# Performance work log

Measured on AMD Instinct MI355X. Metric: run time of the kernel, lower is better.

The kernel has to match this reference:

```python
import jax, jax.numpy as jnp
import numpy as np

K = 10  # neighbors (k = min(k, N-1); N=4096 >> 10)
EPS = 1e-5  # InstanceNorm eps (torch default)


def knn_idx(coords, k):
    # coords: [B,3,N] -> indices of k nearest neighbors (excluding self) [B,N,k]
    pts = coords.transpose(0, 2, 1)  # [B,N,3]
    sq = jnp.sum(pts * pts, axis=-1)  # [B,N]
    dist = sq[:, :, None] + sq[:, None, :] - 2.0 * jnp.einsum('bnc,bmc->bnm', pts, pts)
    dist = jnp.clip(dist, 1e-12)
    _, idx = jax.lax.top_k(-dist, k + 1)  # ascending distance, sorted
    return idx[:, :, 1:]  # drop self


def graph_feature(idx, feats):
    # feats: [B,C,N], idx: [B,N,k] -> [B,2C,N,k] = [center, neighbor-center]
    neigh = jax.vmap(lambda f, i: f[:, i])(feats, idx)  # [B,C,N,k]
    center = jnp.broadcast_to(feats[..., None], neigh.shape)
    return jnp.concatenate([center, neigh - center], axis=1)


def instance_norm(x):
    # x: [B,C,N,k]; normalize over spatial dims per (batch, channel), no affine
    mu = jnp.mean(x, axis=(2, 3), keepdims=True)
    var = jnp.var(x, axis=(2, 3), keepdims=True)
    return (x - mu) * jax.lax.rsqrt(var + EPS)


def lrelu(x):
    return jnp.where(x >= 0, x, 0.2 * x)


def setup_inputs() -> dict:
    key = jax.random.key(0)
    k1, k2, k3, k4, k5 = jax.random.split(key, 5)
    B, C, N = 4, 128, 4096
    coords = jax.random.normal(k1, (B, 3, N), dtype=jnp.float32)
    features = jax.random.normal(k2, (B, C, N), dtype=jnp.float32)
    W1 = jax.random.normal(k3, (C, 2 * C), dtype=jnp.float32) * 0.05
    W2 = jax.random.normal(k4, (2 * C, 2 * C), dtype=jnp.float32) * 0.05
    W3 = jax.random.normal(k5, (C, 4 * C), dtype=jnp.float32) * 0.05
    return {"coords": coords, "features": features, "W1": W1, "W2": W2, "W3": W3}


def reference(coords, features, W1, W2, W3):
    idx = knn_idx(coords, K)  # same KNN graph used by both EdgeConv stages
    x0 = features  # [B,C,N]
    # stage 1: EdgeConv C -> C
    g1 = graph_feature(idx, x0)  # [B,2C,N,k]
    x1 = lrelu(instance_norm(jnp.einsum('oc,bcnk->bonk', W1, g1)))
    x1 = jnp.max(x1, axis=-1)  # [B,C,N]
    # stage 2: EdgeConv C -> 2C
    g2 = graph_feature(idx, x1)  # [B,2C,N,k] (input C, cat -> 2C)
    x2 = lrelu(instance_norm(jnp.einsum('oc,bcnk->bonk', W2, g2)))
    x2 = jnp.max(x2, axis=-1)  # [B,2C,N]
    # fuse: [x0,x1,x2] -> 4C -> C via conv1x1 + InstanceNorm (spatial = N)
    x3 = jnp.concatenate([x0, x1, x2], axis=1)  # [B,4C,N]
    x3 = jnp.einsum('oc,bcn->bon', W3, x3)[..., None]  # [B,C,N,1]
    x3 = lrelu(instance_norm(x3))[..., 0]  # [B,C,N]
    return x3
```

## Files before the change

kernel.cpp:

```cpp
#include <hip/hip_runtime.h>
#include <math.h>
#include <stdint.h>

#define NB 4
#define NC 128
#define NP 4096
#define KNN 10


__device__ __forceinline__ uint16_t f2bf(float f) {
  uint32_t u = __float_as_uint(f);
  u += 0x7fffu + ((u >> 16) & 1u);
  return (uint16_t)(u >> 16);
}
__device__ __forceinline__ float bf2f(uint16_t h) {
  return __uint_as_float(((uint32_t)h) << 16);
}

__device__ __forceinline__ void async16(const void* g, void* l) {
  __builtin_amdgcn_global_load_lds(
      (const __attribute__((address_space(1))) unsigned int*)g,
      (__attribute__((address_space(3))) unsigned int*)l,
      16, 0, 0);
}

__device__ __forceinline__ uint32_t fsort(float f) {
  uint32_t u = __float_as_uint(f);
  return (u & 0x80000000u) ? ~u : (u | 0x80000000u);
}
__device__ __forceinline__ float funsort(uint32_t k) {
  uint32_t u = (k & 0x80000000u) ? (k & 0x7fffffffu) : ~k;
  return __uint_as_float(u);
}

typedef __bf16 bf16x8 __attribute__((ext_vector_type(8)));
typedef float f32x4 __attribute__((ext_vector_type(4)));

__global__ void k_prep(const float* __restrict__ W1, const float* __restrict__ W2,
                       const float* __restrict__ W3, const float* __restrict__ coords,
                       uint16_t* __restrict__ W1cat, uint16_t* __restrict__ W2cat,
                       uint16_t* __restrict__ W3b,
                       float* __restrict__ stats, float4* __restrict__ pts4) {
  int t = blockIdx.x * 256 + threadIdx.x;
  if (t < 32768) {
    int o = t >> 7, c = t & 127;
    float v;
    if (o < 128) v = W1[o * 256 + c] - W1[o * 256 + 128 + c];
    else         v = W1[(o - 128) * 256 + 128 + c];
    W1cat[t] = f2bf(v);
  } else if (t < 98304) {
    int t2 = t - 32768;
    int o = t2 >> 7, c = t2 & 127;
    float v;
    if (o < 256) v = W2[o * 256 + c] - W2[o * 256 + 128 + c];
    else         v = W2[(o - 256) * 256 + 128 + c];
    W2cat[t2] = f2bf(v);
  } else if (t < 163840) {
    int t2 = t - 98304;
    W3b[t2] = f2bf(W3[t2]);
  } else if (t < 163840 + 8192) {
    stats[t - 163840] = 0.f;
  } else if (t < 163840 + 8192 + 16384) {
    int t2 = t - 163840 - 8192;
    int b = t2 >> 12, n = t2 & 4095;
    const float* cb = coords + b * 12288;
    float x = cb[n], y = cb[4096 + n], z = cb[8192 + n];
    float w = fmaf(x, x, fmaf(y, y, z * z));
    pts4[t2] = make_float4(x, y, z, w);
  }
}

__global__ void k_trans_feat(const float* __restrict__ feat, uint16_t* __restrict__ Xcat) {
  __shared__ float tile[32][33];
  int bid = blockIdx.x;
  int b = bid >> 9;
  int r = bid & 511;
  int n0 = (r >> 2) << 5;
  int c0 = (r & 3) << 5;
  int tx = threadIdx.x & 31, ty = threadIdx.x >> 5;
#pragma unroll
  for (int i = 0; i < 4; i++) {
    int c = c0 + ty + i * 8;
    tile[ty + i * 8][tx] = feat[(b * 128 + c) * 4096 + n0 + tx];
  }
  __syncthreads();
#pragma unroll
  for (int i = 0; i < 4; i++) {
    int n = n0 + ty + i * 8;
    Xcat[((b * 4096 + n) * 512) + c0 + tx] = f2bf(tile[tx][ty + i * 8]);
  }
}

__global__ void k_knn_thr(const float4* __restrict__ pts4, float* __restrict__ candd) {
  int L = blockIdx.x;
  int ch = L & 7;
  int qb = (L >> 3) & 15;
  int b = L >> 7;
  int m0 = ch << 7;
  const float4* pb = pts4 + b * 4096;
  int t = threadIdx.x;
  int q = (qb << 8) + t;
  float4 qp = pb[q];
  float d10[10];
#pragma unroll
  for (int i = 0; i < 10; i++) d10[i] = 1e30f;
#pragma unroll 2
  for (int mm = 0; mm < 128; mm++) {
    int m = m0 + mm;
    float4 p = pb[m];
    float dot = fmaf(qp.x, p.x, fmaf(qp.y, p.y, qp.z * p.z));
    float s = qp.w + p.w;
    float d = fmaf(-2.f, dot, s);
    d = (m == q) ? 1e30f : d;
    if (d < d10[9]) {
      float carry = d;
#pragma unroll
      for (int i = 0; i < 10; i++) {
        float lo = fminf(d10[i], carry);
        carry = fmaxf(d10[i], carry);
        d10[i] = lo;
      }
    }
  }
  int row = b * 4096 + q;
#pragma unroll
  for (int i = 0; i < 10; i++) candd[row * 80 + ch * 10 + i] = d10[i];
}

__global__ void k_knn_merge(const float* __restrict__ candd, float* __restrict__ tq) {
  int gw = blockIdx.x * 4 + (threadIdx.x >> 6);
  int l = threadIdx.x & 63;
  const float* cp = candd + (size_t)gw * 80;
  uint32_t k0 = fsort(cp[l]);
  uint32_t k1 = (l < 16) ? fsort(cp[64 + l]) : 0xFFFFFFFFu;
  uint32_t g = 0;
#pragma unroll
  for (int it = 0; it < 10; it++) {
    uint32_t m = k0 < k1 ? k0 : k1;
#pragma unroll
    for (int s = 1; s < 64; s <<= 1) {
      uint32_t o = __shfl_xor(m, s);
      m = o < m ? o : m;
    }
    g = m;
    if (it < 9) {
      if (k0 == m) k0 = 0xFFFFFFFFu;
      else if (k1 == m) k1 = 0xFFFFFFFFu;
    }
  }
  if (l == 0) tq[gw] = funsort(g);
}

#define CFCAP 112
#define DMARGIN 1e-3f
__global__ __launch_bounds__(256) void k_knn_cf(
    const float4* __restrict__ pts4, const float* __restrict__ tq,
    int* __restrict__ idxout) {
  __shared__ int candi[8 * CFCAP];
  __shared__ int ccnt[8];
  int blk = blockIdx.x;
  int b = blk >> 9;
  int qg = blk & 511;
  int t = threadIdx.x;
  if (t < 8) ccnt[t] = 0;
  const float4* pb = pts4 + b * 4096;
  int qbase = qg * 8;
  float q2x[8], q2y[8], q2z[8], rhs[8];
#pragma unroll
  for (int j = 0; j < 8; j++) {
    float4 qp = pb[qbase + j];
    q2x[j] = -2.f * qp.x; q2y[j] = -2.f * qp.y; q2z[j] = -2.f * qp.z;
    rhs[j] = tq[b * 4096 + qbase + j] + DMARGIN - qp.w;
  }
  __syncthreads();
#pragma unroll 4
  for (int c = 0; c < 16; c++) {
    float4 p = pb[c * 256 + t];
    int m = c * 256 + t;
#pragma unroll
    for (int j = 0; j < 8; j++) {
      float tt = fmaf(q2x[j], p.x, fmaf(q2y[j], p.y, fmaf(q2z[j], p.z, p.w)));
      if (tt <= rhs[j]) {
        int pos = atomicAdd(&ccnt[j], 1);
        if (pos < CFCAP) candi[j * CFCAP + pos] = m;
      }
    }
  }
  __syncthreads();
  int w = t >> 6;
  int l = t & 63;
  for (int k = 0; k < 2; k++) {
    int qloc = w * 2 + k;
    int q2 = qbase + qloc;
    float4 qp2 = pb[q2];
    int c = ccnt[qloc]; c = c < CFCAP ? c : CFCAP;
    unsigned long long k0 = ~0ULL, k1 = ~0ULL;
#pragma unroll
    for (int u = 0; u < 2; u++) {
      int j = u * 64 + l;
      if (j < c) {
        int m = candi[qloc * CFCAP + j];
        float4 p = pb[m];
        float dot = fmaf(qp2.x, p.x, fmaf(qp2.y, p.y, qp2.z * p.z));
        float s = qp2.w + p.w;
        float d = fmaf(-2.f, dot, s);
        d = (m == q2) ? 1e30f : d;
        unsigned long long key = (((unsigned long long)fsort(d)) << 32) | (uint32_t)m;
        if (u == 0) k0 = key; else k1 = key;
      }
    }
    uint32_t keep[10];
#pragma unroll
    for (int it = 0; it < 10; it++) {
      unsigned long long m = k0 < k1 ? k0 : k1;
#pragma unroll
      for (int s = 1; s < 64; s <<= 1) {
        unsigned long long o = __shfl_xor(m, s);
        m = o < m ? o : m;
      }
      keep[it] = (uint32_t)(m & 0xffffffffu);
      if (k0 == m) k0 = ~0ULL;
      else if (k1 == m) k1 = ~0ULL;
    }
    if (l == 0) {
      int orow = b * 4096 + q2;
#pragma unroll
      for (int i = 0; i < 10; i++) idxout[orow * 10 + i] = (int)keep[i];
    }
  }
}

__global__ __launch_bounds__(256) void k_gemm_bf(
    const uint16_t* __restrict__ Xb, int ldx, int xoff,
    const uint16_t* __restrict__ Wb, int ldw, int K,
    uint16_t* __restrict__ Ub, uint16_t* __restrict__ Vb,
    int voff, int uld, int vld) {
  __shared__ __align__(16) uint8_t lds[49152];
  const int t = threadIdx.x;
  const int l = t & 63;
  const int wid = t >> 6;
  const int wr = wid & 1, wc = wid >> 1;
  const int p0 = blockIdx.x * 128;
  const int o0 = blockIdx.y * 64;

  const int rA = l >> 3;
  const int cbp = ((l & 7) ^ rA) << 4;
  const int swl = (l & 7) << 4;

  f32x4 acc[4][2];
#pragma unroll
  for (int mi = 0; mi < 4; mi++)
#pragma unroll
    for (int ni = 0; ni < 2; ni++) acc[mi][ni] = (f32x4)0.f;

  auto stage = [&](int k0, int buf) {
    const uint16_t* Xs_ = Xb + (size_t)p0 * ldx + xoff + k0;
    const uint16_t* Ws_ = Wb + (size_t)o0 * ldw + k0;
#pragma unroll
    for (int cc = 0; cc < 4; cc++) {
      int c = wid * 4 + cc;
      const uint8_t* g = (const uint8_t*)(Xs_ + (size_t)(c * 8 + rA) * ldx) + cbp;
      async16(g, &lds[buf * 16384 + c * 1024]);
    }
#pragma unroll
    for (int cc = 0; cc < 2; cc++) {
      int c = wid * 2 + cc;
      const uint8_t* g = (const uint8_t*)(Ws_ + (size_t)(c * 8 + rA) * ldw) + cbp;
      async16(g, &lds[32768 + buf * 8192 + c * 1024]);
    }
  };

  auto compute = [&](int buf) {
    const uint8_t* Ab = &lds[buf * 16384];
    const uint8_t* Bb = &lds[32768 + buf * 8192];
#pragma unroll
    for (int ks = 0; ks < 2; ks++) {
      int cb = ks * 64 + ((l >> 4) << 4);
      bf16x8 bfr[2];
#pragma unroll
      for (int ni = 0; ni < 2; ni++) {
        int n = wc * 32 + ni * 16 + (l & 15);
        bfr[ni] = *(const bf16x8*)(Bb + n * 128 + (cb ^ swl));
      }
#pragma unroll
      for (int mi = 0; mi < 4; mi++) {
        int m = wr * 64 + mi * 16 + (l & 15);
        bf16x8 afr = *(const bf16x8*)(Ab + m * 128 + (cb ^ swl));
        acc[mi][0] = __builtin_amdgcn_mfma_f32_16x16x32_bf16(afr, bfr[0], acc[mi][0], 0, 0, 0);
        acc[mi][1] = __builtin_amdgcn_mfma_f32_16x16x32_bf16(afr, bfr[1], acc[mi][1], 0, 0, 0);
      }
    }
  };

  const int nsteps = K >> 6;
  stage(0, 0);
  for (int s = 0; s < nsteps; s++) {
    __syncthreads();
    if (s + 1 < nsteps) stage((s + 1) << 6, (s + 1) & 1);
    compute(s & 1);
  }

  const bool isv = (o0 >= voff);
#pragma unroll
  for (int mi = 0; mi < 4; mi++)
#pragma unroll
    for (int ni = 0; ni < 2; ni++) {
      int col = o0 + wc * 32 + ni * 16 + (l & 15);
      int row0 = p0 + wr * 64 + mi * 16 + (l >> 4) * 4;
#pragma unroll
      for (int j = 0; j < 4; j++) {
        if (isv) Vb[(size_t)(row0 + j) * vld + (col - voff)] = f2bf(acc[mi][ni][j]);
        else     Ub[(size_t)(row0 + j) * uld + col] = f2bf(acc[mi][ni][j]);
      }
    }
}

__global__ __launch_bounds__(256) void k_gemm3(
    const uint16_t* __restrict__ Xb, int ldx,
    const uint16_t* __restrict__ Wb, int ldw,
    float* __restrict__ Y, int ldy, int K,
    float* __restrict__ T1s, float* __restrict__ T2s) {
  __shared__ __align__(16) uint8_t lds[32768];
  const int t = threadIdx.x;
  const int l = t & 63;
  const int wid = t >> 6;
  const int p0 = blockIdx.x * 64;
  const int o0 = blockIdx.y * 64;

  const int rA = l >> 3;
  const int cbp = ((l & 7) ^ rA) << 4;
  const int swl = (l & 7) << 4;

  f32x4 acc[4];
#pragma unroll
  for (int mi = 0; mi < 4; mi++) acc[mi] = (f32x4)0.f;

  auto stage = [&](int k0, int buf) {
    const uint16_t* Xs_ = Xb + (size_t)p0 * ldx + k0;
    const uint16_t* Ws_ = Wb + (size_t)o0 * ldw + k0;
#pragma unroll
    for (int cc = 0; cc < 2; cc++) {
      int c = wid * 2 + cc;
      const uint8_t* g = (const uint8_t*)(Xs_ + (size_t)(c * 8 + rA) * ldx) + cbp;
      async16(g, &lds[buf * 16384 + c * 1024]);
    }
#pragma unroll
    for (int cc = 0; cc < 2; cc++) {
      int c = wid * 2 + cc;
      const uint8_t* g = (const uint8_t*)(Ws_ + (size_t)(c * 8 + rA) * ldw) + cbp;
      async16(g, &lds[buf * 16384 + 8192 + c * 1024]);
    }
  };

  auto compute = [&](int buf) {
    const uint8_t* Ab = &lds[buf * 16384];
    const uint8_t* Bb = &lds[buf * 16384 + 8192];
#pragma unroll
    for (int ks = 0; ks < 2; ks++) {
      int cb = ks * 64 + ((l >> 4) << 4);
      int n = wid * 16 + (l & 15);
      bf16x8 bfr = *(const bf16x8*)(Bb + n * 128 + (cb ^ swl));
#pragma unroll
      for (int mi = 0; mi < 4; mi++) {
        int m = mi * 16 + (l & 15);
        bf16x8 afr = *(const bf16x8*)(Ab + m * 128 + (cb ^ swl));
        acc[mi] = __builtin_amdgcn_mfma_f32_16x16x32_bf16(afr, bfr, acc[mi], 0, 0, 0);
      }
    }
  };

  const int nsteps = K >> 6;
  stage(0, 0);
  for (int s = 0; s < nsteps; s++) {
    __syncthreads();
    if (s + 1 < nsteps) stage((s + 1) << 6, (s + 1) & 1);
    compute(s & 1);
  }

  int col = o0 + wid * 16 + (l & 15);
#pragma unroll
  for (int mi = 0; mi < 4; mi++) {
    int row0 = p0 + mi * 16 + (l >> 4) * 4;
#pragma unroll
    for (int j = 0; j < 4; j++)
      Y[(size_t)(row0 + j) * ldy + col] = acc[mi][j];
  }
  int b = p0 >> 12;
  float a1 = 0.f, a2 = 0.f;
#pragma unroll
  for (int mi = 0; mi < 4; mi++)
#pragma unroll
    for (int j = 0; j < 4; j++) {
      float y = acc[mi][j];
      a1 += y;
      a2 = fmaf(y, y, a2);
    }
  a1 += __shfl_xor(a1, 16); a2 += __shfl_xor(a2, 16);
  a1 += __shfl_xor(a1, 32); a2 += __shfl_xor(a2, 32);
  if ((l >> 4) == 0) {
    atomicAdd(&T1s[b * 128 + col], a1);
    atomicAdd(&T2s[b * 128 + col], a2);
  }
}

template <int O>
__global__ void k_gather(const uint16_t* __restrict__ Ub,
                         const uint16_t* __restrict__ Vb,
                         const int* __restrict__ idx,
                         uint16_t* __restrict__ S,
                         float* __restrict__ T1, float* __restrict__ T2) {
  int L = blockIdx.x;
  int rx = L & 7;
  int b = rx >> 1;
  int j = ((L >> 3) << 1) + (rx & 1);
  int n0 = j << 4;
  int o = threadIdx.x;
  float a1 = 0.f, a2 = 0.f;
  for (int pi = 0; pi < 16; pi++) {
    int row = b * 4096 + n0 + pi;
    float u = bf2f(Ub[(size_t)row * O + o]);
    float s1 = 0.f, s2 = 0.f, vmax = -1e30f;
#pragma unroll
    for (int jj = 0; jj < KNN; jj++) {
      int m = idx[row * 10 + jj];
      float v = bf2f(Vb[(size_t)(b * 4096 + m) * O + o]);
      s1 += v;
      float x = u + v;
      s2 = fmaf(x, x, s2);
      vmax = fmaxf(vmax, v);
    }
    S[(size_t)row * O + o] = f2bf(u + vmax);
    a1 += 10.f * u + s1;
    a2 += s2;
  }
  atomicAdd(&T1[b * O + o], a1);
  atomicAdd(&T2[b * O + o], a2);
}

template <int O>
__global__ void k_passB(const uint16_t* __restrict__ S, int coff,
                        const float* __restrict__ T1, const float* __restrict__ T2,
                        uint16_t* __restrict__ Xcat) {
  int t = blockIdx.x * 256 + threadIdx.x;
  int o = t & (O - 1);
  int pn = t / O;
  int b = pn >> 12;
  float mu = T1[b * O + o] * (1.f / 40960.f);
  float e2 = T2[b * O + o] * (1.f / 40960.f);
  float inv = rsqrtf(e2 - mu * mu + 1e-5f);
  float x = (bf2f(S[(size_t)pn * O + o]) - mu) * inv;
  Xcat[pn * 512 + coff + o] = f2bf(x >= 0.f ? x : 0.2f * x);
}

__global__ void k_out(const float* __restrict__ Y3, const float* __restrict__ T1,
                      const float* __restrict__ T2, float* __restrict__ out) {
  __shared__ float tile[32][33];
  int bid = blockIdx.x;
  int b = bid >> 9;
  int r = bid & 511;
  int n0 = (r >> 2) << 5;
  int o0 = (r & 3) << 5;
  int tx = threadIdx.x & 31, ty = threadIdx.x >> 5;
  int o = o0 + tx;
  float mu = T1[b * 128 + o] * (1.f / 4096.f);
  float e2 = T2[b * 128 + o] * (1.f / 4096.f);
  float inv = rsqrtf(e2 - mu * mu + 1e-5f);
#pragma unroll
  for (int i = 0; i < 4; i++) {
    int n = n0 + ty + i * 8;
    float v = (Y3[(b * 4096 + n) * 128 + o] - mu) * inv;
    tile[ty + i * 8][tx] = v >= 0.f ? v : 0.2f * v;
  }
  __syncthreads();
#pragma unroll
  for (int i = 0; i < 4; i++) {
    int oo = o0 + ty + i * 8;
    out[(b * 128 + oo) * 4096 + n0 + tx] = tile[tx][ty + i * 8];
  }
}

extern "C" void kernel_launch(void* const* d_in, const int* in_sizes, int n_in,
                              void* d_out, int out_size, void* d_ws, size_t ws_size,
                              hipStream_t stream) {
  const float* coords   = (const float*)d_in[0];
  const float* features = (const float*)d_in[1];
  const float* W1       = (const float*)d_in[2];
  const float* W2       = (const float*)d_in[3];
  const float* W3       = (const float*)d_in[4];
  float* out = (float*)d_out;

  float*    ws    = (float*)d_ws;
  uint16_t* Xcat  = (uint16_t*)ws;
  float*    candd = ws + 4194304;
  float*    tq    = ws + 5505024;
  float4*   pts4  = (float4*)(ws + 5521408);
  uint16_t* Ub1   = (uint16_t*)(ws + 5586944);
  uint16_t* Ub2   = (uint16_t*)(ws + 6635520);
  uint16_t* Sbuf  = (uint16_t*)(ws + 12582912);
  float*    Y3    = ws + 14680064;
  int*      idxb  = (int*)(ws + 16777216);
  uint16_t* W1cat = (uint16_t*)(ws + 16941056);
  uint16_t* W2cat = (uint16_t*)(ws + 16957440);
  uint16_t* W3b   = (uint16_t*)(ws + 16990208);
  float*    stats = ws + 17022976;
  uint16_t* Vb1   = (uint16_t*)(ws + 17031168);
  uint16_t* Vb2   = (uint16_t*)(ws + 18079744);

  k_prep<<<736, 256, 0, stream>>>(W1, W2, W3, coords, W1cat, W2cat, W3b, stats, pts4);
  k_trans_feat<<<2048, 256, 0, stream>>>(features, Xcat);
  k_knn_thr<<<512, 256, 0, stream>>>(pts4, candd);
  k_knn_merge<<<4096, 256, 0, stream>>>(candd, tq);
  k_knn_cf<<<2048, 256, 0, stream>>>(pts4, tq, idxb);

  k_gemm_bf<<<dim3(128, 4), 256, 0, stream>>>(Xcat, 512, 0, W1cat, 128, 128,
                                              Ub1, Vb1, 128, 128, 128);
  k_gather<128><<<1024, 128, 0, stream>>>(Ub1, Vb1, idxb, Sbuf, stats + 0, stats + 512);
  k_passB<128><<<8192, 256, 0, stream>>>(Sbuf, 128, stats + 0, stats + 512, Xcat);

  k_gemm_bf<<<dim3(128, 8), 256, 0, stream>>>(Xcat, 512, 128, W2cat, 128, 128,
                                              Ub2, Vb2, 256, 256, 256);
  k_gather<256><<<1024, 256, 0, stream>>>(Ub2, Vb2, idxb, Sbuf, stats + 1024, stats + 2048);
  k_passB<256><<<16384, 256, 0, stream>>>(Sbuf, 256, stats + 1024, stats + 2048, Xcat);

  k_gemm3<<<dim3(256, 2), 256, 0, stream>>>(Xcat, 512, W3b, 512, Y3, 128, 512,
                                            stats + 3072, stats + 3584);
  k_out<<<2048, 256, 0, stream>>>(Y3, stats + 3072, stats + 3584, out);
}
```

Baseline: 159.1 us.

## Fuse feature transpose into prep kernel and cache candidate distances in KNN filter

Result: no change. 160.0 us (+0.5%).

```diff
diff --git a/kernel.cpp b/kernel.cpp
--- a/kernel.cpp
+++ b/kernel.cpp
@@ -38,10 +38,33 @@
 
 __global__ void k_prep(const float* __restrict__ W1, const float* __restrict__ W2,
                        const float* __restrict__ W3, const float* __restrict__ coords,
+                       const float* __restrict__ feat,
+                       uint16_t* __restrict__ Xcat,
                        uint16_t* __restrict__ W1cat, uint16_t* __restrict__ W2cat,
                        uint16_t* __restrict__ W3b,
                        float* __restrict__ stats, float4* __restrict__ pts4) {
-  int t = blockIdx.x * 256 + threadIdx.x;
+  __shared__ float tile[32][33];
+  int bid = blockIdx.x;
+  if (bid < 2048) {
+    int b = bid >> 9;
+    int r = bid & 511;
+    int n0 = (r >> 2) << 5;
+    int c0 = (r & 3) << 5;
+    int tx = threadIdx.x & 31, ty = threadIdx.x >> 5;
+#pragma unroll
+    for (int i = 0; i < 4; i++) {
+      int c = c0 + ty + i * 8;
+      tile[ty + i * 8][tx] = feat[(b * 128 + c) * 4096 + n0 + tx];
+    }
+    __syncthreads();
+#pragma unroll
+    for (int i = 0; i < 4; i++) {
+      int n = n0 + ty + i * 8;
+      Xcat[((b * 4096 + n) * 512) + c0 + tx] = f2bf(tile[tx][ty + i * 8]);
+    }
+    return;
+  }
+  int t = (bid - 2048) * 256 + threadIdx.x;
   if (t < 32768) {
     int o = t >> 7, c = t & 127;
     float v;
@@ -70,27 +93,6 @@
   }
 }
 
-__global__ void k_trans_feat(const float* __restrict__ feat, uint16_t* __restrict__ Xcat) {
-  __shared__ float tile[32][33];
-  int bid = blockIdx.x;
-  int b = bid >> 9;
-  int r = bid & 511;
-  int n0 = (r >> 2) << 5;
-  int c0 = (r & 3) << 5;
-  int tx = threadIdx.x & 31, ty = threadIdx.x >> 5;
-#pragma unroll
-  for (int i = 0; i < 4; i++) {
-    int c = c0 + ty + i * 8;
-    tile[ty + i * 8][tx] = feat[(b * 128 + c) * 4096 + n0 + tx];
-  }
-  __syncthreads();
-#pragma unroll
-  for (int i = 0; i < 4; i++) {
-    int n = n0 + ty + i * 8;
-    Xcat[((b * 4096 + n) * 512) + c0 + tx] = f2bf(tile[tx][ty + i * 8]);
-  }
-}
-
 __global__ void k_knn_thr(const float4* __restrict__ pts4, float* __restrict__ candd) {
   int L = blockIdx.x;
   int ch = L & 7;
@@ -156,6 +158,7 @@
 __global__ __launch_bounds__(256) void k_knn_cf(
     const float4* __restrict__ pts4, const float* __restrict__ tq,
     int* __restrict__ idxout) {
+  __shared__ float cdd[8 * CFCAP];
   __shared__ int candi[8 * CFCAP];
   __shared__ int ccnt[8];
   int blk = blockIdx.x;
@@ -165,11 +168,12 @@
   if (t < 8) ccnt[t] = 0;
   const float4* pb = pts4 + b * 4096;
   int qbase = qg * 8;
-  float q2x[8], q2y[8], q2z[8], rhs[8];
+  float q2x[8], q2y[8], q2z[8], qw[8], rhs[8];
 #pragma unroll
   for (int j = 0; j < 8; j++) {
     float4 qp = pb[qbase + j];
     q2x[j] = -2.f * qp.x; q2y[j] = -2.f * qp.y; q2z[j] = -2.f * qp.z;
+    qw[j] = qp.w;
     rhs[j] = tq[b * 4096 + qbase + j] + DMARGIN - qp.w;
   }
   __syncthreads();
@@ -181,8 +185,11 @@
     for (int j = 0; j < 8; j++) {
       float tt = fmaf(q2x[j], p.x, fmaf(q2y[j], p.y, fmaf(q2z[j], p.z, p.w)));
       if (tt <= rhs[j]) {
+        float qx = -0.5f * q2x[j], qy = -0.5f * q2y[j], qz = -0.5f * q2z[j];
+        float dot = fmaf(qx, p.x, fmaf(qy, p.y, qz * p.z));
+        float d = fmaf(-2.f, dot, qw[j] + p.w);
         int pos = atomicAdd(&ccnt[j], 1);
-        if (pos < CFCAP) candi[j * CFCAP + pos] = m;
+        if (pos < CFCAP) { cdd[j * CFCAP + pos] = d; candi[j * CFCAP + pos] = m; }
       }
     }
   }
@@ -192,40 +199,43 @@
   for (int k = 0; k < 2; k++) {
     int qloc = w * 2 + k;
     int q2 = qbase + qloc;
-    float4 qp2 = pb[q2];
     int c = ccnt[qloc]; c = c < CFCAP ? c : CFCAP;
-    unsigned long long k0 = ~0ULL, k1 = ~0ULL;
-#pragma unroll
-    for (int u = 0; u < 2; u++) {
-      int j = u * 64 + l;
-      if (j < c) {
-        int m = candi[qloc * CFCAP + j];
-        float4 p = pb[m];
-        float dot = fmaf(qp2.x, p.x, fmaf(qp2.y, p.y, qp2.z * p.z));
-        float s = qp2.w + p.w;
-        float d = fmaf(-2.f, dot, s);
-        d = (m == q2) ? 1e30f : d;
-        unsigned long long key = (((unsigned long long)fsort(d)) << 32) | (uint32_t)m;
-        if (u == 0) k0 = key; else k1 = key;
-      }
-    }
-    uint32_t keep[10];
+    float d0 = 1e30f, d1 = 1e30f; int i0 = 0x7fffffff, i1 = 0x7fffffff;
+    if (l < c)      { d0 = cdd[qloc * CFCAP + l];      i0 = candi[qloc * CFCAP + l];
+                      if (i0 == q2) d0 = 1e30f; }
+    if (64 + l < c) { d1 = cdd[qloc * CFCAP + 64 + l]; i1 = candi[qloc * CFCAP + 64 + l];
+                      if (i1 == q2) d1 = 1e30f; }
+    uint32_t k0 = fsort(d0), k1 = fsort(d1);
+    int orow = b * 4096 + q2;
 #pragma unroll
     for (int it = 0; it < 10; it++) {
-      unsigned long long m = k0 < k1 ? k0 : k1;
+      uint32_t m = k0 < k1 ? k0 : k1;
 #pragma unroll
       for (int s = 1; s < 64; s <<= 1) {
-        unsigned long long o = __shfl_xor(m, s);
+        uint32_t o = __shfl_xor(m, s);
         m = o < m ? o : m;
       }
-      keep[it] = (uint32_t)(m & 0xffffffffu);
-      if (k0 == m) k0 = ~0ULL;
-      else if (k1 == m) k1 = ~0ULL;
-    }
-    if (l == 0) {
-      int orow = b * 4096 + q2;
-#pragma unroll
-      for (int i = 0; i < 10; i++) idxout[orow * 10 + i] = (int)keep[i];
+      int li = 0x7fffffff, ls = -1;
+      if (k0 == m) { li = i0; ls = 0; }
+      if (k1 == m && i1 < li) { li = i1; ls = 1; }
+      unsigned long long bal = __ballot(ls >= 0);
+      int winner;
+      if (__popcll(bal) == 1) {
+        winner = __ffsll(bal) - 1;
+      } else {
+        int mi = (ls >= 0) ? li : 0x7fffffff;
+#pragma unroll
+        for (int s = 1; s < 64; s <<= 1) {
+          int o = __shfl_xor(mi, s);
+          mi = o < mi ? o : mi;
+        }
+        unsigned long long b2 = __ballot(ls >= 0 && li == mi);
+        winner = __ffsll(b2) - 1;
+      }
+      if (l == winner) {
+        idxout[orow * 10 + it] = li;
+        if (ls == 0) k0 = 0xFFFFFFFFu; else k1 = 0xFFFFFFFFu;
+      }
     }
   }
 }
@@ -506,8 +516,8 @@
   uint16_t* Vb1   = (uint16_t*)(ws + 17031168);
   uint16_t* Vb2   = (uint16_t*)(ws + 18079744);
 
-  k_prep<<<736, 256, 0, stream>>>(W1, W2, W3, coords, W1cat, W2cat, W3b, stats, pts4);
-  k_trans_feat<<<2048, 256, 0, stream>>>(features, Xcat);
+  k_prep<<<2784, 256, 0, stream>>>(W1, W2, W3, coords, features, Xcat,
+                                   W1cat, W2cat, W3b, stats, pts4);
   k_knn_thr<<<512, 256, 0, stream>>>(pts4, candd);
   k_knn_merge<<<4096, 256, 0, stream>>>(candd, tq);
   k_knn_cf<<<2048, 256, 0, stream>>>(pts4, tq, idxb);
```
